# Kernel tuning notes

Hardware: AMD Instinct MI355X
Metric: run time of the kernel (lower is better)

Reference implementation:

```python
import jax, jax.numpy as jnp
import numpy as np

B, S, HID = 1, 2048, 2048
NUM_HEADS, NUM_KV_HEADS, HEAD_DIM = 16, 4, 128
ROPE_THETA = 10000.0
EPS = 1e-6


def setup_inputs() -> dict:
    key = jax.random.key(0)
    ks = jax.random.split(key, 9)
    s = 0.02
    return {
        "hidden_states": jax.random.normal(ks[0], (B, S, HID), jnp.float32),
        "mu_prev": jax.random.normal(ks[1], (B, S, HID), jnp.float32),
        "wq": jax.random.normal(ks[2], (NUM_HEADS * HEAD_DIM, HID), jnp.float32) * s,
        "wk": jax.random.normal(ks[3], (NUM_KV_HEADS * HEAD_DIM, HID), jnp.float32) * s,
        "wv": jax.random.normal(ks[4], (NUM_KV_HEADS * HEAD_DIM, HID), jnp.float32) * s,
        "wo": jax.random.normal(ks[5], (HID, NUM_HEADS * HEAD_DIM), jnp.float32) * s,
        "wmq": jax.random.normal(ks[6], (NUM_HEADS * HEAD_DIM, HID), jnp.float32) * (s * 0.1),
        "wmk": jax.random.normal(ks[7], (NUM_KV_HEADS * HEAD_DIM, HID), jnp.float32) * (s * 0.1),
        "wmv": jax.random.normal(ks[8], (NUM_KV_HEADS * HEAD_DIM, HID), jnp.float32) * (s * 0.1),
        "q_norm_w": jnp.ones((HEAD_DIM,), jnp.float32),
        "k_norm_w": jnp.ones((HEAD_DIM,), jnp.float32),
    }


def _rmsnorm(x, w):
    var = jnp.mean(jnp.square(x), axis=-1, keepdims=True)
    return x * jax.lax.rsqrt(var + EPS) * w


def _rope_cos_sin(seq_len, dtype):
    inv_freq = 1.0 / (ROPE_THETA ** (jnp.arange(0, HEAD_DIM, 2, dtype=jnp.float32) / HEAD_DIM))
    freqs = jnp.arange(seq_len, dtype=jnp.float32)[:, None] * inv_freq[None, :]  # [S, D/2]
    emb = jnp.concatenate([freqs, freqs], axis=-1)  # [S, D]
    return jnp.cos(emb).astype(dtype), jnp.sin(emb).astype(dtype)


def _rotate_half(x):
    x1, x2 = jnp.split(x, 2, axis=-1)
    return jnp.concatenate([-x2, x1], axis=-1)


def reference(hidden_states, mu_prev, wq, wk, wv, wo, wmq, wmk, wmv, q_norm_w, k_norm_w):
    b, s, _ = hidden_states.shape
    # Fused mu-guided QKV projections (cat(x, mu) @ cat(W, Wm)^T == x@W^T + mu@Wm^T)
    q = hidden_states @ wq.T + mu_prev @ wmq.T  # [B,S,H*D]
    k = hidden_states @ wk.T + mu_prev @ wmk.T  # [B,S,KV*D]
    v = hidden_states @ wv.T + mu_prev @ wmv.T
    q = q.reshape(b, s, NUM_HEADS, HEAD_DIM).transpose(0, 2, 1, 3)      # [B,H,S,D]
    k = k.reshape(b, s, NUM_KV_HEADS, HEAD_DIM).transpose(0, 2, 1, 3)   # [B,KV,S,D]
    v = v.reshape(b, s, NUM_KV_HEADS, HEAD_DIM).transpose(0, 2, 1, 3)
    # per-head QK RMSNorm
    q = _rmsnorm(q, q_norm_w)
    k = _rmsnorm(k, k_norm_w)
    # RoPE
    cos, sin = _rope_cos_sin(s, q.dtype)
    q = q * cos + _rotate_half(q) * sin
    k = k * cos + _rotate_half(k) * sin
    # GQA attention without materializing repeated K/V: group query heads
    g = NUM_HEADS // NUM_KV_HEADS
    qg = q.reshape(b, NUM_KV_HEADS, g, s, HEAD_DIM)
    scale = 1.0 / jnp.sqrt(jnp.asarray(HEAD_DIM, q.dtype))
    scores = jnp.einsum('bkgqd,bkld->bkgql', qg, k) * scale  # [B,KV,G,S,S]
    causal = jnp.tril(jnp.ones((s, s), bool))
    scores = jnp.where(causal, scores, jnp.asarray(-jnp.inf, scores.dtype))
    probs = jax.nn.softmax(scores.astype(jnp.float32), axis=-1).astype(q.dtype)
    out = jnp.einsum('bkgql,bkld->bkgqd', probs, v)  # [B,KV,G,S,D]
    out = out.reshape(b, NUM_HEADS, s, HEAD_DIM).transpose(0, 2, 1, 3).reshape(b, s, NUM_HEADS * HEAD_DIM)
    return out @ wo.T
```

## Files before the change

### kernel.cpp

```cpp
#include <hip/hip_runtime.h>
#include <math.h>

#define SEQ 2048
#define HID_DIM 2048
#define NH 16
#define NKV 4
#define HD 128
#define QS 3072

typedef float  f4v  __attribute__((ext_vector_type(4)));
typedef __bf16 bf8v __attribute__((ext_vector_type(8)));
typedef __bf16 bf4v __attribute__((ext_vector_type(4)));
typedef __bf16 bf2v __attribute__((ext_vector_type(2)));

typedef __attribute__((address_space(1))) const void* gvp;
typedef __attribute__((address_space(3))) void*       svp;

__device__ __forceinline__ void gld16(const void* g, void* lds_wave_base) {
    __builtin_amdgcn_global_load_lds((gvp)g, (svp)lds_wave_base, 16, 0, 0);
}

__global__ __launch_bounds__(256)
void cvt_cat2(__bf16* __restrict__ dst, const float* __restrict__ s0,
              const float* __restrict__ s1, int rows, int kq)
{
    int i = blockIdx.x * 256 + threadIdx.x;
    if (i >= rows * kq * 2) return;
    int row = i / (2 * kq), c = i - row * 2 * kq;
    const float* s = (c < kq) ? s0 + ((size_t)row * kq + c) * 4
                              : s1 + ((size_t)row * kq + (c - kq)) * 4;
    float4 v = *reinterpret_cast<const float4*>(s);
    *reinterpret_cast<bf4v*>(dst + ((size_t)row * 2 * kq + c) * 4) =
        bf4v{ (__bf16)v.x, (__bf16)v.y, (__bf16)v.z, (__bf16)v.w };
}

__global__ __launch_bounds__(256)
void cvt(__bf16* __restrict__ dst, const float* __restrict__ src, int n4)
{
    int i = blockIdx.x * 256 + threadIdx.x;
    if (i >= n4) return;
    float4 v = *reinterpret_cast<const float4*>(src + (size_t)i * 4);
    *reinterpret_cast<bf4v*>(dst + (size_t)i * 4) =
        bf4v{ (__bf16)v.x, (__bf16)v.y, (__bf16)v.z, (__bf16)v.w };
}

__global__ __launch_bounds__(256)
void gemm_nt_sp(const __bf16* __restrict__ A, const __bf16* __restrict__ B,
                __bf16* __restrict__ P, int M, int N, int K, int KS)
{
    __shared__ __bf16 As[128 * 32];
    __shared__ __bf16 Bs[128 * 32];
    const int tid = threadIdx.x, lane = tid & 63, w = tid >> 6;
    const int wm = w >> 1, wn = w & 1;
    const int mm = lane & 15, quad = lane >> 4;
    const int m0 = blockIdx.y * 128, n0 = blockIdx.x * 128;
    const int kz0 = blockIdx.z * KS;
    const int r0 = lane >> 2, c0 = (lane & 3) * 8;

    f4v acc[4][4] = {};

    for (int k0 = kz0; k0 < kz0 + KS; k0 += 32) {
#pragma unroll
        for (int j = 0; j < 2; ++j) {
            int chunk = w * 2 + j;
            int row   = chunk * 16 + r0;
            gld16(&A[(size_t)(m0 + row) * K + k0 + c0], (char*)As + chunk * 1024);
            gld16(&B[(size_t)(n0 + row) * K + k0 + c0], (char*)Bs + chunk * 1024);
        }
        __syncthreads();
        bf8v af[4], bfv[4];
#pragma unroll
        for (int t = 0; t < 4; ++t) {
            af[t]  = *reinterpret_cast<const bf8v*>(&As[(wm * 64 + t * 16 + mm) * 32 + quad * 8]);
            bfv[t] = *reinterpret_cast<const bf8v*>(&Bs[(wn * 64 + t * 16 + mm) * 32 + quad * 8]);
        }
#pragma unroll
        for (int mt = 0; mt < 4; ++mt)
#pragma unroll
            for (int nt = 0; nt < 4; ++nt)
                acc[mt][nt] = __builtin_amdgcn_mfma_f32_16x16x32_bf16(af[mt], bfv[nt], acc[mt][nt], 0, 0, 0);
        __syncthreads();
    }
    __bf16* Pz = P + (size_t)blockIdx.z * M * N;
#pragma unroll
    for (int mt = 0; mt < 4; ++mt)
#pragma unroll
        for (int nt = 0; nt < 4; ++nt)
#pragma unroll
            for (int r = 0; r < 4; ++r)
                Pz[(size_t)(m0 + wm * 64 + mt * 16 + quad * 4 + r) * N
                   + n0 + wn * 64 + nt * 16 + mm] = (__bf16)acc[mt][nt][r];
}

__global__ __launch_bounds__(256)
void add4(const __bf16* __restrict__ P, float* __restrict__ out, int n4)
{
    int i = blockIdx.x * 256 + threadIdx.x;
    if (i >= n4) return;
    float4 s = {0.f, 0.f, 0.f, 0.f};
#pragma unroll
    for (int z = 0; z < 4; ++z) {
        bf4v v = *reinterpret_cast<const bf4v*>(P + (size_t)z * n4 * 4 + (size_t)i * 4);
        s.x += (float)v[0]; s.y += (float)v[1]; s.z += (float)v[2]; s.w += (float)v[3];
    }
    *reinterpret_cast<float4*>(out + (size_t)i * 4) = s;
}

__global__ __launch_bounds__(64)
void norm_rope(__bf16* __restrict__ qkv ,
               const __bf16* __restrict__ p1,
               const float* __restrict__ qw, const float* __restrict__ kw)
{
    const int s = blockIdx.x, hh = blockIdx.y, l = threadIdx.x;
    const float* wn; float scale; int off;
    if (hh < NH) { off = hh * HD;               wn = qw; scale = 0.08838834764831845f; }
    else         { off = 2048 + (hh - NH) * HD; wn = kw; scale = 1.0f; }
    __bf16* p = qkv + (size_t)s * QS + off;
    const __bf16* q1 = p1 + (size_t)s * QS + off;
    float x0 = (float)p[l]      + (float)q1[l];
    float x1 = (float)p[l + 64] + (float)q1[l + 64];
    float ss = x0 * x0 + x1 * x1;
#pragma unroll
    for (int o = 32; o; o >>= 1) ss += __shfl_xor(ss, o);
    float inv = rsqrtf(ss * (1.0f / 128.0f) + 1e-6f);
    x0 *= inv * wn[l];
    x1 *= inv * wn[l + 64];
    float invf = exp2f(-(float)l * (13.287712379549449f / 64.0f));
    float ang  = (float)s * invf;
    float c, sn;
    sincosf(ang, &sn, &c);
    p[l]      = (__bf16)((x0 * c - x1 * sn) * scale);
    p[l + 64] = (__bf16)((x1 * c + x0 * sn) * scale);
}

__global__ __launch_bounds__(256)
void pack_k(const __bf16* __restrict__ qkv, __bf16* __restrict__ Kt)
{
    const int kt = blockIdx.x, kh = blockIdx.y, t = threadIdx.x;
    char* tile = (char*)Kt + ((size_t)(kh * 32 + kt)) * 16384;
    const __bf16* src = qkv + 2048 + kh * HD;
#pragma unroll
    for (int i = 0; i < 4; ++i) {
        int cid = t * 4 + i;
        int key = cid >> 4, pc = cid & 15;
        int c = pc ^ (key & 15);
        bf8v v = *reinterpret_cast<const bf8v*>(src + (size_t)(kt * 64 + key) * QS + c * 8);
        *reinterpret_cast<bf8v*>(tile + cid * 16) = v;
    }
}

__global__ __launch_bounds__(256)
void pack_v(const __bf16* __restrict__ qkv0, const __bf16* __restrict__ qkv1,
            __bf16* __restrict__ Vt)
{
    const int kt = blockIdx.x, kh = blockIdx.y, t = threadIdx.x;
    char* tile = (char*)Vt + ((size_t)(kh * 32 + kt)) * 16384;
    const __bf16* s0 = qkv0 + 2560 + kh * HD;
    const __bf16* s1 = qkv1 + 2560 + kh * HD;
#pragma unroll
    for (int i = 0; i < 4; ++i) {
        int cid = t * 4 + i;
        int d = cid >> 3, kcp = cid & 7;
        int kc = kcp ^ (d & 7);
        size_t base = (size_t)(kt * 64 + kc * 8) * QS + d;
        __bf16 tmp[8];
#pragma unroll
        for (int j = 0; j < 8; ++j)
            tmp[j] = (__bf16)((float)s0[base + (size_t)j * QS] +
                              (float)s1[base + (size_t)j * QS]);
        *reinterpret_cast<bf8v*>(tile + cid * 16) = *reinterpret_cast<bf8v*>(tmp);
    }
}

__global__ __launch_bounds__(256)
void attn_split(const __bf16* __restrict__ qkv,
                const __bf16* __restrict__ Kt, const __bf16* __restrict__ Vt,
                __bf16* __restrict__ Op, float* __restrict__ Lp)
{
    __shared__ char Ks[16384];
    __shared__ char Vs[16384];
    __shared__ char Ps[4][2048];

    const int c = blockIdx.x, qt = 31 - blockIdx.y, h = blockIdx.z;
    if (c * 8 > qt) return;
    const int kend = min(qt, c * 8 + 7);
    const int tid = threadIdx.x, lane = tid & 63, w = tid >> 6;
    const int mm = lane & 15, quad = lane >> 4;
    const int kh = h >> 2;

    bf8v aq[4];
    const __bf16* qbase = qkv + (size_t)(qt * 64 + w * 16 + mm) * QS + h * HD;
#pragma unroll
    for (int ks = 0; ks < 4; ++ks)
        aq[ks] = *reinterpret_cast<const bf8v*>(qbase + ks * 32 + quad * 8);

    float lp[4] = {};
    f4v oacc[8] = {};

    for (int kt = c * 8; kt <= kend; ++kt) {
        __syncthreads();
        const char* ktile = (const char*)Kt + ((size_t)(kh * 32 + kt)) * 16384;
        const char* vtile = (const char*)Vt + ((size_t)(kh * 32 + kt)) * 16384;
#pragma unroll
        for (int j = 0; j < 4; ++j) {
            int chunk = w * 4 + j;
            gld16(ktile + chunk * 1024 + lane * 16, Ks + chunk * 1024);
            gld16(vtile + chunk * 1024 + lane * 16, Vs + chunk * 1024);
        }
        __syncthreads();

        f4v s[4] = {};
#pragma unroll
        for (int ks = 0; ks < 4; ++ks)
#pragma unroll
            for (int c16 = 0; c16 < 4; ++c16) {
                bf8v b = *reinterpret_cast<const bf8v*>(
                    Ks + (c16 * 16 + mm) * 256 + (((ks * 4 + quad) ^ mm) << 4));
                s[c16] = __builtin_amdgcn_mfma_f32_16x16x32_bf16(aq[ks], b, s[c16], 0, 0, 0);
            }
        if (kt == qt) {
#pragma unroll
            for (int c16 = 0; c16 < 4; ++c16)
#pragma unroll
                for (int r = 0; r < 4; ++r)
                    if (c16 * 16 + mm > w * 16 + quad * 4 + r)
                        s[c16][r] = -__builtin_inff();
        }
        float pr[4][4];
#pragma unroll
        for (int c16 = 0; c16 < 4; ++c16)
#pragma unroll
            for (int r = 0; r < 4; ++r) {
                pr[c16][r] = __expf(s[c16][r]);
                lp[r] += pr[c16][r];
            }
#pragma unroll
        for (int c16 = 0; c16 < 4; ++c16)
#pragma unroll
            for (int r = 0; r < 4; ++r) {
                float mine  = pr[c16][r];
                float other = __shfl_xor(mine, 1);
                if ((mm & 1) == 0) {
                    int roww = quad * 4 + r;
                    int cc   = c16 * 2 + (mm >> 3);
                    *reinterpret_cast<bf2v*>(
                        &Ps[w][roww * 128 + ((cc ^ (roww & 7)) << 4) + (mm & 7) * 2]) =
                        bf2v{ (__bf16)mine, (__bf16)other };
                }
            }
        bf8v pa[2];
#pragma unroll
        for (int kb = 0; kb < 2; ++kb)
            pa[kb] = *reinterpret_cast<const bf8v*>(
                &Ps[w][mm * 128 + (((kb * 4 + quad) ^ (mm & 7)) << 4)]);
#pragma unroll
        for (int nb = 0; nb < 8; ++nb) {
            int d = nb * 16 + mm;
#pragma unroll
            for (int kb = 0; kb < 2; ++kb) {
                bf8v bv = *reinterpret_cast<const bf8v*>(
                    Vs + d * 128 + (((kb * 4 + quad) ^ (d & 7)) << 4));
                oacc[nb] = __builtin_amdgcn_mfma_f32_16x16x32_bf16(pa[kb], bv, oacc[nb], 0, 0, 0);
            }
        }
    }
#pragma unroll
    for (int off = 1; off < 16; off <<= 1)
#pragma unroll
        for (int r = 0; r < 4; ++r) lp[r] += __shfl_xor(lp[r], off);
#pragma unroll
    for (int r = 0; r < 4; ++r) {
        int row = qt * 64 + w * 16 + quad * 4 + r;
        size_t obase = ((size_t)(c * 16 + h) * SEQ + row) * HD;
#pragma unroll
        for (int nb = 0; nb < 8; ++nb)
            Op[obase + nb * 16 + mm] = (__bf16)oacc[nb][r];
        if (mm == 0)
            Lp[(size_t)(c * 16 + h) * SEQ + row] = lp[r];
    }
}

__global__ __launch_bounds__(64)
void combine(const __bf16* __restrict__ Op, const float* __restrict__ Lp,
             __bf16* __restrict__ ab)
{
    const int row = blockIdx.x, h = blockIdx.y, l = threadIdx.x;
    const int nch = (row >> 9) + 1;
    float L = 0.f, a0 = 0.f, a1 = 0.f;
    for (int c = 0; c < nch; ++c) {
        L += Lp[(size_t)(c * 16 + h) * SEQ + row];
        bf2v p = *reinterpret_cast<const bf2v*>(
            Op + ((size_t)(c * 16 + h) * SEQ + row) * HD + 2 * l);
        a0 += (float)p[0];
        a1 += (float)p[1];
    }
    float inv = 1.f / L;
    *reinterpret_cast<bf2v*>(ab + (size_t)row * (NH * HD) + h * HD + 2 * l) =
        bf2v{ (__bf16)(a0 * inv), (__bf16)(a1 * inv) };
}

extern "C" void kernel_launch(void* const* d_in, const int* in_sizes, int n_in,
                              void* d_out, int out_size, void* d_ws, size_t ws_size,
                              hipStream_t stream)
{
    const float* hs  = (const float*)d_in[0];
    const float* mu  = (const float*)d_in[1];
    const float* wq  = (const float*)d_in[2];
    const float* wk  = (const float*)d_in[3];
    const float* wv  = (const float*)d_in[4];
    const float* wo  = (const float*)d_in[5];
    const float* wmq = (const float*)d_in[6];
    const float* wmk = (const float*)d_in[7];
    const float* wmv = (const float*)d_in[8];
    const float* qw  = (const float*)d_in[9];
    const float* kw  = (const float*)d_in[10];
    float* out = (float*)d_out;

    char* ws = (char*)d_ws;
    __bf16* Wcat = (__bf16*)(ws + 0);
    __bf16* Acat = (__bf16*)(ws + 25165824);
    __bf16* Wo   = (__bf16*)(ws + 41943040);
    __bf16* qkvp = (__bf16*)(ws + 50331648);
    __bf16* ab   = (__bf16*)(ws + 75497472);
    __bf16* Ktl  = (__bf16*)(ws + 0);
    __bf16* Vtl  = (__bf16*)(ws + 2097152);
    __bf16* Opart= (__bf16*)(ws + 4194304);
    float*  Lpart= (float*) (ws + 37748736);
    __bf16* outp = (__bf16*)(ws + 0);

    cvt_cat2<<<dim3((2048 * 1024 + 255) / 256), 256, 0, stream>>>(Acat, hs, mu, 2048, 512);
    cvt_cat2<<<dim3((2048 * 1024 + 255) / 256), 256, 0, stream>>>(Wcat, wq, wmq, 2048, 512);
    cvt_cat2<<<dim3((512 * 1024 + 255) / 256), 256, 0, stream>>>(Wcat + (size_t)2048 * 4096, wk, wmk, 512, 512);
    cvt_cat2<<<dim3((512 * 1024 + 255) / 256), 256, 0, stream>>>(Wcat + (size_t)2560 * 4096, wv, wmv, 512, 512);
    cvt<<<dim3((1024 * 1024 + 255) / 256), 256, 0, stream>>>(Wo, wo, 1024 * 1024);

    gemm_nt_sp<<<dim3(QS / 128, SEQ / 128, 2), 256, 0, stream>>>(Acat, Wcat, qkvp, SEQ, QS, 2 * HID_DIM, HID_DIM);
    norm_rope<<<dim3(SEQ, NH + NKV), dim3(64), 0, stream>>>(qkvp, qkvp + (size_t)SEQ * QS, qw, kw);
    pack_k<<<dim3(32, NKV), 256, 0, stream>>>(qkvp, Ktl);
    pack_v<<<dim3(32, NKV), 256, 0, stream>>>(qkvp, qkvp + (size_t)SEQ * QS, Vtl);
    attn_split<<<dim3(4, 32, NH), 256, 0, stream>>>(qkvp, Ktl, Vtl, Opart, Lpart);
    combine<<<dim3(SEQ, NH), 64, 0, stream>>>(Opart, Lpart, ab);
    gemm_nt_sp<<<dim3(HID_DIM / 128, SEQ / 128, 4), 256, 0, stream>>>(ab, Wo, outp, SEQ, HID_DIM, NH * HD, 512);
    add4<<<dim3((1024 * 1024 + 255) / 256), 256, 0, stream>>>(outp, out, 1024 * 1024);
}
```

Before: 367.4 us.

## Double-buffer K/V tiles in attention and fuse conversion kernels into one launch

The attention kernel now uses two LDS buffers for K and V, so the next tile's global-to-LDS load is issued while the current tile is being computed. This hides load latency behind MFMA work and removes one barrier per iteration, at the cost of doubling LDS use to about 72KB per block, which may lower occupancy. The five fp32-to-bf16 conversion launches are merged into a single kernel to cut launch overhead. The GEMM also gains a clamp on the K range.

New measurement: 371.8 us. Within noise of the previous version (+1.2%).

```diff
diff --git a/kernel.cpp b/kernel.cpp
--- a/kernel.cpp
+++ b/kernel.cpp
@@ -20,12 +20,9 @@
     __builtin_amdgcn_global_load_lds((gvp)g, (svp)lds_wave_base, 16, 0, 0);
 }
 
-__global__ __launch_bounds__(256)
-void cvt_cat2(__bf16* __restrict__ dst, const float* __restrict__ s0,
-              const float* __restrict__ s1, int rows, int kq)
-{
-    int i = blockIdx.x * 256 + threadIdx.x;
-    if (i >= rows * kq * 2) return;
+__device__ __forceinline__ void cat2_item(__bf16* dst, const float* s0,
+                                          const float* s1, int i, int kq)
+{
     int row = i / (2 * kq), c = i - row * 2 * kq;
     const float* s = (c < kq) ? s0 + ((size_t)row * kq + c) * 4
                               : s1 + ((size_t)row * kq + (c - kq)) * 4;
@@ -35,13 +32,25 @@
 }
 
 __global__ __launch_bounds__(256)
-void cvt(__bf16* __restrict__ dst, const float* __restrict__ src, int n4)
+void cvt_all(const float* __restrict__ hs, const float* __restrict__ mu,
+             const float* __restrict__ wq, const float* __restrict__ wmq,
+             const float* __restrict__ wk, const float* __restrict__ wmk,
+             const float* __restrict__ wv, const float* __restrict__ wmv,
+             const float* __restrict__ wo,
+             __bf16* __restrict__ Acat, __bf16* __restrict__ Wcat,
+             __bf16* __restrict__ Wo)
 {
     int i = blockIdx.x * 256 + threadIdx.x;
-    if (i >= n4) return;
-    float4 v = *reinterpret_cast<const float4*>(src + (size_t)i * 4);
-    *reinterpret_cast<bf4v*>(dst + (size_t)i * 4) =
-        bf4v{ (__bf16)v.x, (__bf16)v.y, (__bf16)v.z, (__bf16)v.w };
+    if (i < 2097152)       cat2_item(Acat, hs, mu, i, 512);
+    else if (i < 4194304)  cat2_item(Wcat, wq, wmq, i - 2097152, 512);
+    else if (i < 4718592)  cat2_item(Wcat + (size_t)2048 * 4096, wk, wmk, i - 4194304, 512);
+    else if (i < 5242880)  cat2_item(Wcat + (size_t)2560 * 4096, wv, wmv, i - 4718592, 512);
+    else if (i < 6291456) {
+        int j = i - 5242880;
+        float4 v = *reinterpret_cast<const float4*>(wo + (size_t)j * 4);
+        *reinterpret_cast<bf4v*>(Wo + (size_t)j * 4) =
+            bf4v{ (__bf16)v.x, (__bf16)v.y, (__bf16)v.z, (__bf16)v.w };
+    }
 }
 
 __global__ __launch_bounds__(256)
@@ -55,11 +64,12 @@
     const int mm = lane & 15, quad = lane >> 4;
     const int m0 = blockIdx.y * 128, n0 = blockIdx.x * 128;
     const int kz0 = blockIdx.z * KS;
+    const int kEnd = min(kz0 + KS, K);
     const int r0 = lane >> 2, c0 = (lane & 3) * 8;
 
     f4v acc[4][4] = {};
 
-    for (int k0 = kz0; k0 < kz0 + KS; k0 += 32) {
+    for (int k0 = kz0; k0 < kEnd; k0 += 32) {
 #pragma unroll
         for (int j = 0; j < 2; ++j) {
             int chunk = w * 2 + j;
@@ -177,13 +187,13 @@
                 const __bf16* __restrict__ Kt, const __bf16* __restrict__ Vt,
                 __bf16* __restrict__ Op, float* __restrict__ Lp)
 {
-    __shared__ char Ks[16384];
-    __shared__ char Vs[16384];
+    __shared__ char Ks[2][16384];
+    __shared__ char Vs[2][16384];
     __shared__ char Ps[4][2048];
 
     const int c = blockIdx.x, qt = 31 - blockIdx.y, h = blockIdx.z;
     if (c * 8 > qt) return;
-    const int kend = min(qt, c * 8 + 7);
+    const int kbeg = c * 8, kend = min(qt, c * 8 + 7);
     const int tid = threadIdx.x, lane = tid & 63, w = tid >> 6;
     const int mm = lane & 15, quad = lane >> 4;
     const int kh = h >> 2;
@@ -197,17 +207,31 @@
     float lp[4] = {};
     f4v oacc[8] = {};
 
-    for (int kt = c * 8; kt <= kend; ++kt) {
-        __syncthreads();
-        const char* ktile = (const char*)Kt + ((size_t)(kh * 32 + kt)) * 16384;
-        const char* vtile = (const char*)Vt + ((size_t)(kh * 32 + kt)) * 16384;
+    {
+        const char* ktile = (const char*)Kt + ((size_t)(kh * 32 + kbeg)) * 16384;
+        const char* vtile = (const char*)Vt + ((size_t)(kh * 32 + kbeg)) * 16384;
 #pragma unroll
         for (int j = 0; j < 4; ++j) {
             int chunk = w * 4 + j;
-            gld16(ktile + chunk * 1024 + lane * 16, Ks + chunk * 1024);
-            gld16(vtile + chunk * 1024 + lane * 16, Vs + chunk * 1024);
-        }
+            gld16(ktile + chunk * 1024 + lane * 16, Ks[0] + chunk * 1024);
+            gld16(vtile + chunk * 1024 + lane * 16, Vs[0] + chunk * 1024);
+        }
+    }
+    int cur = 0;
+    for (int kt = kbeg; kt <= kend; ++kt) {
         __syncthreads();
+        if (kt < kend) {
+            const char* ktile = (const char*)Kt + ((size_t)(kh * 32 + kt + 1)) * 16384;
+            const char* vtile = (const char*)Vt + ((size_t)(kh * 32 + kt + 1)) * 16384;
+#pragma unroll
+            for (int j = 0; j < 4; ++j) {
+                int chunk = w * 4 + j;
+                gld16(ktile + chunk * 1024 + lane * 16, Ks[cur ^ 1] + chunk * 1024);
+                gld16(vtile + chunk * 1024 + lane * 16, Vs[cur ^ 1] + chunk * 1024);
+            }
+        }
+        const char* KsC = Ks[cur];
+        const char* VsC = Vs[cur];
 
         f4v s[4] = {};
 #pragma unroll
@@ -215,7 +239,7 @@
 #pragma unroll
             for (int c16 = 0; c16 < 4; ++c16) {
                 bf8v b = *reinterpret_cast<const bf8v*>(
-                    Ks + (c16 * 16 + mm) * 256 + (((ks * 4 + quad) ^ mm) << 4));
+                    KsC + (c16 * 16 + mm) * 256 + (((ks * 4 + quad) ^ mm) << 4));
                 s[c16] = __builtin_amdgcn_mfma_f32_16x16x32_bf16(aq[ks], b, s[c16], 0, 0, 0);
             }
         if (kt == qt) {
@@ -259,10 +283,11 @@
 #pragma unroll
             for (int kb = 0; kb < 2; ++kb) {
                 bf8v bv = *reinterpret_cast<const bf8v*>(
-                    Vs + d * 128 + (((kb * 4 + quad) ^ (d & 7)) << 4));
+                    VsC + d * 128 + (((kb * 4 + quad) ^ (d & 7)) << 4));
                 oacc[nb] = __builtin_amdgcn_mfma_f32_16x16x32_bf16(pa[kb], bv, oacc[nb], 0, 0, 0);
             }
         }
+        cur ^= 1;
     }
 #pragma unroll
     for (int off = 1; off < 16; off <<= 1)
@@ -322,22 +347,20 @@
     __bf16* Wo   = (__bf16*)(ws + 41943040);
     __bf16* qkvp = (__bf16*)(ws + 50331648);
     __bf16* ab   = (__bf16*)(ws + 75497472);
+    const size_t QKVN = (size_t)SEQ * QS;
     __bf16* Ktl  = (__bf16*)(ws + 0);
     __bf16* Vtl  = (__bf16*)(ws + 2097152);
     __bf16* Opart= (__bf16*)(ws + 4194304);
     float*  Lpart= (float*) (ws + 37748736);
     __bf16* outp = (__bf16*)(ws + 0);
 
-    cvt_cat2<<<dim3((2048 * 1024 + 255) / 256), 256, 0, stream>>>(Acat, hs, mu, 2048, 512);
-    cvt_cat2<<<dim3((2048 * 1024 + 255) / 256), 256, 0, stream>>>(Wcat, wq, wmq, 2048, 512);
-    cvt_cat2<<<dim3((512 * 1024 + 255) / 256), 256, 0, stream>>>(Wcat + (size_t)2048 * 4096, wk, wmk, 512, 512);
-    cvt_cat2<<<dim3((512 * 1024 + 255) / 256), 256, 0, stream>>>(Wcat + (size_t)2560 * 4096, wv, wmv, 512, 512);
-    cvt<<<dim3((1024 * 1024 + 255) / 256), 256, 0, stream>>>(Wo, wo, 1024 * 1024);
+    cvt_all<<<dim3(24576), 256, 0, stream>>>(hs, mu, wq, wmq, wk, wmk, wv, wmv, wo,
+                                             Acat, Wcat, Wo);
 
     gemm_nt_sp<<<dim3(QS / 128, SEQ / 128, 2), 256, 0, stream>>>(Acat, Wcat, qkvp, SEQ, QS, 2 * HID_DIM, HID_DIM);
-    norm_rope<<<dim3(SEQ, NH + NKV), dim3(64), 0, stream>>>(qkvp, qkvp + (size_t)SEQ * QS, qw, kw);
+    norm_rope<<<dim3(SEQ, NH + NKV), dim3(64), 0, stream>>>(qkvp, qkvp + QKVN, qw, kw);
     pack_k<<<dim3(32, NKV), 256, 0, stream>>>(qkvp, Ktl);
-    pack_v<<<dim3(32, NKV), 256, 0, stream>>>(qkvp, qkvp + (size_t)SEQ * QS, Vtl);
+    pack_v<<<dim3(32, NKV), 256, 0, stream>>>(qkvp, qkvp + QKVN, Vtl);
     attn_split<<<dim3(4, 32, NH), 256, 0, stream>>>(qkvp, Ktl, Vtl, Opart, Lpart);
     combine<<<dim3(SEQ, NH), 64, 0, stream>>>(Opart, Lpart, ab);
     gemm_nt_sp<<<dim3(HID_DIM / 128, SEQ / 128, 4), 256, 0, stream>>>(ab, Wo, outp, SEQ, HID_DIM, NH * HD, 512);
```
